# Performance work log

Measured on AMD Instinct MI355X. Metric: run time of the kernel, lower is better.

## Reference

```python
import jax, jax.numpy as jnp
from jax import lax
import numpy as np

EPS = 1e-5

def setup_inputs() -> dict:
    key = jax.random.key(0)
    k1, k2, k3, k4 = jax.random.split(key, 4)
    B, in_c, out_c, k, z_dim, H, W = 16, 128, 256, 3, 256, 64, 64
    fan_in = in_c * k * k
    x = jax.random.normal(k1, (B, in_c, H, W), dtype=jnp.float32)
    z = jax.random.normal(k2, (B, z_dim), dtype=jnp.float32)
    base_weight = jax.random.normal(k3, (out_c, in_c, k, k), dtype=jnp.float32) * np.sqrt(2.0 / fan_in)
    head_w = jax.random.normal(k4, (out_c * in_c * k * k, z_dim), dtype=jnp.float32) * np.sqrt(1.0 / z_dim)
    return {"x": x, "z": z, "base_weight": base_weight, "head_w": head_w}

def reference(x, z, base_weight, head_w):
    # x: [B, in_c, H, W]; z: [B, z_dim]; base_weight: [out_c, in_c, k, k]; head_w: [out_c*in_c*k*k, z_dim]
    B = x.shape[0]
    out_c, in_c, k, _ = base_weight.shape
    fan_in = in_c * k * k
    hyper_weight = 1.0

    # delta_w = Linear(z) -> [B, out_c, in_c, k, k]
    delta_w = jnp.einsum('bz,oz->bo', z, head_w).reshape(B, out_c, in_c, k, k)
    # standardize over (in_c, k, k) per (sample, out-channel)
    mu = jnp.mean(delta_w, axis=(2, 3, 4), keepdims=True)
    var = jnp.var(delta_w, axis=(2, 3, 4), keepdims=True)
    delta_w = (delta_w - mu) * lax.rsqrt(var + EPS)
    delta_w = delta_w * jnp.sqrt(2.0 / fan_in)

    w = (base_weight[None] + hyper_weight * delta_w) / jnp.sqrt(2.0)  # [B, out_c, in_c, k, k]

    pad = k // 2
    def conv_one(xb, wb):
        # xb: [in_c, H, W], wb: [out_c, in_c, k, k]
        return lax.conv_general_dilated(
            xb[None], wb, window_strides=(1, 1), padding=[(pad, pad), (pad, pad)],
            dimension_numbers=('NCHW', 'OIHW', 'NCHW'))[0]

    out = jax.vmap(conv_one)(x, w)  # [B, out_c, H_out, W_out]
    return out
```

## Files before the change

kernel.cpp:

```cpp
#include <hip/hip_runtime.h>

#define B_  16
#define IC  128
#define OC  256
#define ZD  256
#define HH  64
#define WW  64
#define FAN 1152
#define NO  294912
#define HP  66

typedef float    fvec4 __attribute__((ext_vector_type(4)));
typedef _Float16 f16x8 __attribute__((ext_vector_type(8)));
typedef _Float16 f16x4 __attribute__((ext_vector_type(4)));

__device__ __forceinline__ void gl_lds16(const _Float16* g, _Float16* ldst) {
  __builtin_amdgcn_global_load_lds(
      (const __attribute__((address_space(1))) unsigned int*)(const void*)g,
      (__attribute__((address_space(3))) unsigned int*)(void*)ldst,
      16, 0, 0);
}

__global__ __launch_bounds__(256) void delta_gemm_kernel(
    const float* __restrict__ z, const float* __restrict__ head_w,
    float* __restrict__ delta) {
  __shared__ _Float16 As[256 * 72];
  __shared__ _Float16 zsh[16 * 264];
  int t = threadIdx.x;
  int row0 = blockIdx.x * 256;
  int lane = t & 63, wave = t >> 6;
  int quad = lane >> 4, l16 = lane & 15;

  for (int u = t; u < 1024; u += 256) {
    int b = u >> 6, kq = u & 63;
    fvec4 v = *(const fvec4*)&z[b * 256 + kq * 4];
    f16x4 h = {(_Float16)v.x, (_Float16)v.y, (_Float16)v.z, (_Float16)v.w};
    *(f16x4*)&zsh[b * 264 + kq * 4] = h;
  }

  fvec4 acc[4];
#pragma unroll
  for (int i = 0; i < 4; ++i) acc[i] = (fvec4){0.f, 0.f, 0.f, 0.f};

  int srow_lo = t >> 4;
  int sseg = t & 15;

  for (int zc2 = 0; zc2 < 4; ++zc2) {
    __syncthreads();
#pragma unroll
    for (int i = 0; i < 16; ++i) {
      int row = i * 16 + srow_lo;
      fvec4 v = *(const fvec4*)&head_w[(size_t)(row0 + row) * 256 + zc2 * 64 + sseg * 4];
      f16x4 h = {(_Float16)v.x, (_Float16)v.y, (_Float16)v.z, (_Float16)v.w};
      *(f16x4*)&As[row * 72 + sseg * 4] = h;
    }
    __syncthreads();
#pragma unroll
    for (int kc = 0; kc < 2; ++kc) {
      f16x8 bfz = *(const f16x8*)&zsh[l16 * 264 + zc2 * 64 + kc * 32 + quad * 8];
#pragma unroll
      for (int mt = 0; mt < 4; ++mt) {
        f16x8 af = *(const f16x8*)&As[(wave * 64 + mt * 16 + l16) * 72 + kc * 32 + quad * 8];
        acc[mt] = __builtin_amdgcn_mfma_f32_16x16x32_f16(af, bfz, acc[mt], 0, 0, 0);
      }
    }
  }
#pragma unroll
  for (int mt = 0; mt < 4; ++mt) {
    int gr = row0 + wave * 64 + mt * 16 + quad * 4;
#pragma unroll
    for (int r = 0; r < 4; ++r)
      delta[(size_t)l16 * NO + gr + r] = acc[mt][r];
  }
}

__global__ __launch_bounds__(256) void standardize_kernel(
    const float* __restrict__ delta, const float* __restrict__ base_w,
    _Float16* __restrict__ w_h) {
  int b  = blockIdx.x >> 8;
  int oc = blockIdx.x & 255;
  int tid = threadIdx.x;
  const float* d = delta + (size_t)b * NO + oc * FAN;

  float s = 0.f, s2 = 0.f;
  for (int j = tid; j < FAN; j += 256) { float v = d[j]; s += v; s2 += v * v; }
#pragma unroll
  for (int off = 32; off > 0; off >>= 1) {
    s  += __shfl_down(s, off);
    s2 += __shfl_down(s2, off);
  }
  __shared__ float rs[4], rq[4];
  if ((tid & 63) == 0) { rs[tid >> 6] = s; rq[tid >> 6] = s2; }
  __syncthreads();
  float S  = rs[0] + rs[1] + rs[2] + rs[3];
  float S2 = rq[0] + rq[1] + rq[2] + rq[3];
  const float inv_fan = 1.0f / (float)FAN;
  float mu  = S * inv_fan;
  float var = S2 * inv_fan - mu * mu;
  const float inv_sqrt2 = 0.70710678118654752f;
  float sc = rsqrtf(var + 1e-5f) * sqrtf(2.0f / (float)FAN) * inv_sqrt2;

  const float* bw = base_w + oc * FAN;
  _Float16* wp = w_h + ((size_t)b * OC + oc) * FAN;
  for (int i = tid; i < FAN; i += 256) {
    int ic = i & 127, kk = i >> 7;
    int j = ic * 9 + kk;
    float val = bw[j] * inv_sqrt2 + (d[j] - mu) * sc;
    wp[i] = (_Float16)val;
  }
}

__global__ __launch_bounds__(256) void xpose_kernel(
    const float* __restrict__ x, _Float16* __restrict__ x_h) {
  int yp = blockIdx.x;
  int b  = blockIdx.y;
  int t  = threadIdx.x;
  _Float16* orow = x_h + ((size_t)(b * HP + yp)) * HP * IC;

  if (yp == 0 || yp == HP - 1) {
    fvec4 zz = (fvec4){0.f, 0.f, 0.f, 0.f};
    for (int u = t; u < HP * IC / 8; u += 256)
      ((fvec4*)orow)[u] = zz;
    return;
  }
  int y = yp - 1;
  __shared__ float tile[128 * 65];
#pragma unroll
  for (int i = 0; i < 8; ++i) {
    int F = i * 256 + t;
    int ic = F >> 4, xq = F & 15;
    fvec4 v = *(const fvec4*)&x[(((size_t)b * IC + ic) * HH + y) * WW + xq * 4];
    float* tp = &tile[ic * 65 + xq * 4];
    tp[0] = v.x; tp[1] = v.y; tp[2] = v.z; tp[3] = v.w;
  }
  __syncthreads();
#pragma unroll
  for (int j = 0; j < 4; ++j) {
    int u = j * 256 + t;
    int px = u >> 4, icg = u & 15;
    _Float16 h[8];
#pragma unroll
    for (int c = 0; c < 8; ++c) h[c] = (_Float16)tile[(icg * 8 + c) * 65 + px];
    *(f16x8*)&orow[(px + 1) * IC + icg * 8] = *(f16x8*)h;
  }
  if (t < 32) {
    int side = t >> 4, icg = t & 15;
    fvec4 zz = (fvec4){0.f, 0.f, 0.f, 0.f};
    *(fvec4*)&orow[(side ? (HP - 1) * IC : 0) + icg * 8] = zz;
  }
}

__global__ __launch_bounds__(256) void conv_mfma_kernel(
    const _Float16* __restrict__ x_h, const _Float16* __restrict__ w_h,
    float* __restrict__ out) {
  __shared__ __align__(16) _Float16 As[128 * 64];
  __shared__ __align__(16) _Float16 Bs[128 * 64];
  int t = threadIdx.x;
  int b = blockIdx.z;
  int oc0 = blockIdx.y * 128;
  int y0 = blockIdx.x * 2;
  int lane = t & 63, wave = t >> 6;
  int wm = wave >> 1, wn = wave & 1;
  int quad = lane >> 4, l16 = lane & 15;

  fvec4 acc[4][4];
#pragma unroll
  for (int i = 0; i < 4; ++i)
#pragma unroll
    for (int j = 0; j < 4; ++j) acc[i][j] = (fvec4){0.f, 0.f, 0.f, 0.f};

  int lrow = lane >> 3;
  int lseg = lane & 7;
  int sw   = lseg ^ lrow;

  const _Float16* apg[4];
#pragma unroll
  for (int n = 0; n < 4; ++n)
    apg[n] = w_h + ((size_t)(b * OC + oc0 + wave * 32 + n * 8 + lrow)) * FAN + sw * 8;

  const _Float16* bpg0 =
      x_h + (((size_t)(b * HP + y0 + (wave >> 1))) * HP + (wave & 1) * 32 + lrow) * IC + sw * 8;
  const _Float16* bpg1 = bpg0 + 16 * IC;

  _Float16* adst = As + wave * 32 * 64;
  _Float16* bdst = Bs + wave * 32 * 64;

  int s7 = l16 & 7;
  int arow = (wm * 64 + l16) * 64;
  int brow = (wn * 64 + l16) * 64;
  int aoff[2] = { arow + ((0 + quad) ^ s7) * 8, arow + ((4 + quad) ^ s7) * 8 };
  int boff[2] = { brow + ((0 + quad) ^ s7) * 8, brow + ((4 + quad) ^ s7) * 8 };

#pragma unroll
  for (int ky = 0; ky < 3; ++ky) {
#pragma unroll
    for (int kx = 0; kx < 3; ++kx) {
      const int kk = ky * 3 + kx;
      const _Float16* b0k = bpg0 + (ky * HP + kx) * IC;
      const _Float16* b1k = bpg1 + (ky * HP + kx) * IC;
#pragma unroll
      for (int icc = 0; icc < 2; ++icc) {
        __syncthreads();
#pragma unroll
        for (int n = 0; n < 4; ++n)
          gl_lds16(apg[n] + kk * 128 + icc * 64, adst + n * 512);
        gl_lds16(b0k + icc * 64,        bdst);
        gl_lds16(b0k + 1024 + icc * 64, bdst + 512);
        gl_lds16(b1k + icc * 64,        bdst + 1024);
        gl_lds16(b1k + 1024 + icc * 64, bdst + 1536);
        __syncthreads();
#pragma unroll
        for (int ks = 0; ks < 2; ++ks) {
          f16x8 af[4], bf[4];
#pragma unroll
          for (int i = 0; i < 4; ++i)
            af[i] = *(const f16x8*)&As[aoff[ks] + i * 1024];
#pragma unroll
          for (int j = 0; j < 4; ++j)
            bf[j] = *(const f16x8*)&Bs[boff[ks] + j * 1024];
#pragma unroll
          for (int i = 0; i < 4; ++i)
#pragma unroll
            for (int j = 0; j < 4; ++j)
              acc[i][j] = __builtin_amdgcn_mfma_f32_16x16x32_f16(af[i], bf[j], acc[i][j], 0, 0, 0);
        }
      }
    }
  }

#pragma unroll
  for (int i = 0; i < 4; ++i)
#pragma unroll
    for (int j = 0; j < 4; ++j) {
      int m  = oc0 + wm * 64 + i * 16 + quad * 4;
      int nn = wn * 64 + j * 16 + l16;
      int oy = y0 + (nn >> 6), ox = nn & 63;
      float* op = out + (((size_t)(b * OC + m) * HH + oy) * WW + ox);
#pragma unroll
      for (int r = 0; r < 4; ++r)
        op[(size_t)r * HH * WW] = acc[i][j][r];
    }
}

extern "C" void kernel_launch(void* const* d_in, const int* in_sizes, int n_in,
                              void* d_out, int out_size, void* d_ws, size_t ws_size,
                              hipStream_t stream) {
  const float* x      = (const float*)d_in[0];
  const float* z      = (const float*)d_in[1];
  const float* base_w = (const float*)d_in[2];
  const float* head_w = (const float*)d_in[3];
  float* out = (float*)d_out;

  _Float16* w_h   = (_Float16*)d_ws;
  float*    delta = (float*)((char*)d_ws + (size_t)B_ * OC * FAN * sizeof(_Float16));
  _Float16* x_h   = (_Float16*)((char*)d_ws + (size_t)B_ * OC * FAN * sizeof(_Float16)
                                            + (size_t)B_ * NO * sizeof(float));

  delta_gemm_kernel<<<NO / 256, 256, 0, stream>>>(z, head_w, delta);
  standardize_kernel<<<B_ * OC, 256, 0, stream>>>(delta, base_w, w_h);
  xpose_kernel<<<dim3(HP, B_), 256, 0, stream>>>(x, x_h);
  conv_mfma_kernel<<<dim3(32, 2, B_), 256, 0, stream>>>(x_h, w_h, out);
}
```

Before: 504.7 us.

## Rewrite conv kernel with 4-stage async LDS pipeline and 256x256 tiles

The conv kernel now uses 512 threads and computes a 256-oc by 256-pixel tile per block, with a K step of 32. Global-to-LDS loads are spread over four ring buffers and gated by manual vmcnt waits and a raw s_barrier, so loads are issued several stages ahead of the MFMAs. Wave priority is raised around the MFMA blocks. The aim is to hide memory latency and improve operand reuse. In exchange it uses more registers (32 accumulator tiles) and 128KB of LDS, and the launch grid shrinks to 256 blocks.

```diff
diff --git a/kernel.cpp b/kernel.cpp
--- a/kernel.cpp
+++ b/kernel.cpp
@@ -20,6 +20,12 @@
       (__attribute__((address_space(3))) unsigned int*)(void*)ldst,
       16, 0, 0);
 }
+
+#define BARRIER()  asm volatile("s_barrier" ::: "memory")
+#define WAITVM8()  asm volatile("s_waitcnt vmcnt(8)" ::: "memory")
+#define WAITVM4()  asm volatile("s_waitcnt vmcnt(4)" ::: "memory")
+#define WAITVM0()  asm volatile("s_waitcnt vmcnt(0)" ::: "memory")
+#define WAITLGKM() asm volatile("s_waitcnt lgkmcnt(0)" ::: "memory")
 
 __global__ __launch_bounds__(256) void delta_gemm_kernel(
     const float* __restrict__ z, const float* __restrict__ head_w,
@@ -150,95 +156,118 @@
   }
 }
 
-__global__ __launch_bounds__(256) void conv_mfma_kernel(
+__global__ __launch_bounds__(512, 2) void conv_mfma_kernel(
     const _Float16* __restrict__ x_h, const _Float16* __restrict__ w_h,
     float* __restrict__ out) {
-  __shared__ __align__(16) _Float16 As[128 * 64];
-  __shared__ __align__(16) _Float16 Bs[128 * 64];
-  int t = threadIdx.x;
-  int b = blockIdx.z;
-  int oc0 = blockIdx.y * 128;
-  int y0 = blockIdx.x * 2;
-  int lane = t & 63, wave = t >> 6;
-  int wm = wave >> 1, wn = wave & 1;
-  int quad = lane >> 4, l16 = lane & 15;
-
-  fvec4 acc[4][4];
-#pragma unroll
-  for (int i = 0; i < 4; ++i)
+  __shared__ __align__(16) _Float16 As[4 * 8192];
+  __shared__ __align__(16) _Float16 Bs[4 * 8192];
+  const int t = threadIdx.x;
+  const int b = blockIdx.y;
+  const int y0 = blockIdx.x * 4;
+  const int lane = t & 63, wave = t >> 6;
+  const int wm = wave >> 2, wn = wave & 3;
+  const int quad = lane >> 4, l16 = lane & 15;
+
+  fvec4 acc[8][4];
+#pragma unroll
+  for (int i = 0; i < 8; ++i)
 #pragma unroll
     for (int j = 0; j < 4; ++j) acc[i][j] = (fvec4){0.f, 0.f, 0.f, 0.f};
 
-  int lrow = lane >> 3;
-  int lseg = lane & 7;
-  int sw   = lseg ^ lrow;
-
-  const _Float16* apg[4];
-#pragma unroll
-  for (int n = 0; n < 4; ++n)
-    apg[n] = w_h + ((size_t)(b * OC + oc0 + wave * 32 + n * 8 + lrow)) * FAN + sw * 8;
-
-  const _Float16* bpg0 =
-      x_h + (((size_t)(b * HP + y0 + (wave >> 1))) * HP + (wave & 1) * 32 + lrow) * IC + sw * 8;
-  const _Float16* bpg1 = bpg0 + 16 * IC;
-
-  _Float16* adst = As + wave * 32 * 64;
-  _Float16* bdst = Bs + wave * 32 * 64;
-
-  int s7 = l16 & 7;
-  int arow = (wm * 64 + l16) * 64;
-  int brow = (wn * 64 + l16) * 64;
-  int aoff[2] = { arow + ((0 + quad) ^ s7) * 8, arow + ((4 + quad) ^ s7) * 8 };
-  int boff[2] = { brow + ((0 + quad) ^ s7) * 8, brow + ((4 + quad) ^ s7) * 8 };
-
-#pragma unroll
-  for (int ky = 0; ky < 3; ++ky) {
-#pragma unroll
-    for (int kx = 0; kx < 3; ++kx) {
-      const int kk = ky * 3 + kx;
-      const _Float16* b0k = bpg0 + (ky * HP + kx) * IC;
-      const _Float16* b1k = bpg1 + (ky * HP + kx) * IC;
-#pragma unroll
-      for (int icc = 0; icc < 2; ++icc) {
-        __syncthreads();
-#pragma unroll
-        for (int n = 0; n < 4; ++n)
-          gl_lds16(apg[n] + kk * 128 + icc * 64, adst + n * 512);
-        gl_lds16(b0k + icc * 64,        bdst);
-        gl_lds16(b0k + 1024 + icc * 64, bdst + 512);
-        gl_lds16(b1k + icc * 64,        bdst + 1024);
-        gl_lds16(b1k + 1024 + icc * 64, bdst + 1536);
-        __syncthreads();
-#pragma unroll
-        for (int ks = 0; ks < 2; ++ks) {
-          f16x8 af[4], bf[4];
-#pragma unroll
-          for (int i = 0; i < 4; ++i)
-            af[i] = *(const f16x8*)&As[aoff[ks] + i * 1024];
-#pragma unroll
-          for (int j = 0; j < 4; ++j)
-            bf[j] = *(const f16x8*)&Bs[boff[ks] + j * 1024];
-#pragma unroll
-          for (int i = 0; i < 4; ++i)
-#pragma unroll
-            for (int j = 0; j < 4; ++j)
-              acc[i][j] = __builtin_amdgcn_mfma_f32_16x16x32_f16(af[i], bf[j], acc[i][j], 0, 0, 0);
-        }
-      }
-    }
-  }
-
-#pragma unroll
-  for (int i = 0; i < 4; ++i)
-#pragma unroll
-    for (int j = 0; j < 4; ++j) {
-      int m  = oc0 + wm * 64 + i * 16 + quad * 4;
-      int nn = wn * 64 + j * 16 + l16;
-      int oy = y0 + (nn >> 6), ox = nn & 63;
-      float* op = out + (((size_t)(b * OC + m) * HH + oy) * WW + ox);
+  const int lr  = lane >> 2;
+  const int sw2 = (lane & 3) ^ ((lane >> 2) & 3) ^ ((lane >> 4) & 3);
+
+  const _Float16* apb0 = w_h + ((size_t)(b * OC + wave * 32 + lr)) * FAN + sw2 * 8;
+  const _Float16* apb1 = apb0 + (size_t)16 * FAN;
+  const int p0 = wave * 32 + lr, p1 = p0 + 16;
+  const _Float16* bpb0 =
+      x_h + (((size_t)(b * HP + y0 + (p0 >> 6))) * HP + (p0 & 63)) * IC + sw2 * 8;
+  const _Float16* bpb1 =
+      x_h + (((size_t)(b * HP + y0 + (p1 >> 6))) * HP + (p1 & 63)) * IC + sw2 * 8;
+
+  const int adst = wave * 32 * 32;
+
+  const int xoro = (l16 & 3) ^ ((l16 >> 2) & 3);
+  const int aro = (wm * 128 + l16) * 32 + ((quad ^ xoro) << 3);
+  const int bro = (wn * 64  + l16) * 32 + ((quad ^ xoro) << 3);
+
+#define STAGE(slot, akoff, bkoff)                                   \
+  do {                                                              \
+    _Float16* ad = As + (slot) * 8192 + adst;                       \
+    _Float16* bd = Bs + (slot) * 8192 + adst;                       \
+    gl_lds16(apb0 + (akoff), ad);                                   \
+    gl_lds16(apb1 + (akoff), ad + 512);                             \
+    gl_lds16(bpb0 + (bkoff), bd);                                   \
+    gl_lds16(bpb1 + (bkoff), bd + 512);                             \
+  } while (0)
+
+#define COMPUTE(slot)                                               \
+  do {                                                              \
+    const _Float16* Ab = As + (slot) * 8192;                        \
+    const _Float16* Bb = Bs + (slot) * 8192;                        \
+    f16x8 bf[4];                                                    \
+    _Pragma("unroll")                                               \
+    for (int nf = 0; nf < 4; ++nf)                                  \
+      bf[nf] = *(const f16x8*)&Bb[bro + nf * 512];                  \
+    __builtin_amdgcn_s_setprio(1);                                  \
+    _Pragma("unroll")                                               \
+    for (int mf = 0; mf < 8; ++mf) {                                \
+      f16x8 af = *(const f16x8*)&Ab[aro + mf * 512];                \
+      _Pragma("unroll")                                             \
+      for (int nf = 0; nf < 4; ++nf)                                \
+        acc[mf][nf] =                                               \
+            __builtin_amdgcn_mfma_f32_16x16x32_f16(af, bf[nf], acc[mf][nf], 0, 0, 0); \
+    }                                                               \
+    __builtin_amdgcn_s_setprio(0);                                  \
+  } while (0)
+
+  STAGE(0, 0, 0);
+  STAGE(1, 32, 32);
+  STAGE(2, 64, 64);
+
+  for (int kk = 0; kk < 8; ++kk) {
+    const int ky  = kk / 3,       kx  = kk % 3;
+    const int ky1 = (kk + 1) / 3, kx1 = (kk + 1) % 3;
+    const int ka  = kk * 128;
+    const int kb  = (ky * HP + kx) * IC;
+    const int ka1 = ka + 128;
+    const int kb1 = (ky1 * HP + kx1) * IC;
+#pragma unroll
+    for (int c = 0; c < 4; ++c) {
+      WAITLGKM();
+      WAITVM8();
+      BARRIER();
+      if (c == 0) STAGE(3, ka + 96, kb + 96);
+      else        STAGE(c - 1, ka1 + (c - 1) * 32, kb1 + (c - 1) * 32);
+      COMPUTE(c);
+    }
+  }
+  {
+    const int ka = 1024, kb = (2 * HP + 2) * IC;
+    WAITLGKM(); WAITVM8(); BARRIER();
+    STAGE(3, ka + 96, kb + 96);
+    COMPUTE(0);
+    WAITLGKM(); WAITVM8(); BARRIER();
+    COMPUTE(1);
+    WAITLGKM(); WAITVM4(); BARRIER();
+    COMPUTE(2);
+    WAITLGKM(); WAITVM0(); BARRIER();
+    COMPUTE(3);
+  }
+#undef STAGE
+#undef COMPUTE
+
+#pragma unroll
+  for (int mf = 0; mf < 8; ++mf)
+#pragma unroll
+    for (int nf = 0; nf < 4; ++nf) {
+      int oc = wm * 128 + mf * 16 + quad * 4;
+      int pn = wn * 64 + nf * 16 + l16;
+      int oy = y0 + (pn >> 6), ox = pn & 63;
+      float* op = out + (((size_t)(b * OC + oc) * HH + oy) * WW + ox);
 #pragma unroll
       for (int r = 0; r < 4; ++r)
-        op[(size_t)r * HH * WW] = acc[i][j][r];
+        op[(size_t)r * HH * WW] = acc[mf][nf][r];
     }
 }
 
@@ -259,5 +288,5 @@
   delta_gemm_kernel<<<NO / 256, 256, 0, stream>>>(z, head_w, delta);
   standardize_kernel<<<B_ * OC, 256, 0, stream>>>(delta, base_w, w_h);
   xpose_kernel<<<dim3(HP, B_), 256, 0, stream>>>(x, x_h);
-  conv_mfma_kernel<<<dim3(32, 2, B_), 256, 0, stream>>>(x_h, w_h, out);
-}
+  conv_mfma_kernel<<<dim3(16, B_), 512, 0, stream>>>(x_h, w_h, out);
+}
```

After: 509.5 us. No clear change (+0.9%).

## Fuse hypernetwork delta GEMM with per-channel standardization into one kernel

Applied to the files above, without the earlier changes.

Replaces the separate delta GEMM and standardize kernels with one kernel per output channel. Each block streams its head_w slice with register prefetch and double-buffered LDS, computes delta for all 16 samples via MFMA, reduces mean and variance in registers, and writes the fp16 standardized weights directly. This removes the fp32 delta buffer write and re-read and one launch. In exchange, only 256 large blocks run with heavy LDS use, which may limit memory-level parallelism when streaming head_w.

```diff
diff --git a/kernel.cpp b/kernel.cpp
--- a/kernel.cpp
+++ b/kernel.cpp
@@ -21,92 +21,118 @@
       16, 0, 0);
 }
 
-__global__ __launch_bounds__(256) void delta_gemm_kernel(
+#define BARRIER()  asm volatile("s_barrier" ::: "memory")
+#define WAITLGKM() asm volatile("s_waitcnt lgkmcnt(0)" ::: "memory")
+
+__global__ __launch_bounds__(512) void delta_std_fused_kernel(
     const float* __restrict__ z, const float* __restrict__ head_w,
-    float* __restrict__ delta) {
-  __shared__ _Float16 As[256 * 72];
+    const float* __restrict__ base_w, _Float16* __restrict__ w_h) {
+  __shared__ __align__(16) _Float16 As2[2][128 * 264];
   __shared__ _Float16 zsh[16 * 264];
-  int t = threadIdx.x;
-  int row0 = blockIdx.x * 256;
-  int lane = t & 63, wave = t >> 6;
-  int quad = lane >> 4, l16 = lane & 15;
-
-  for (int u = t; u < 1024; u += 256) {
+  __shared__ float bsh[FAN];
+  __shared__ float swS[8 * 16], swQ[8 * 16];
+  __shared__ float musb[16], scb[16];
+
+  const int t = threadIdx.x;
+  const int oc = blockIdx.x;
+  const int lane = t & 63, wave = t >> 6;
+  const int quad = lane >> 4, l16 = lane & 15;
+
+  const float* hw = head_w + (size_t)oc * FAN * ZD;
+  const float* hwp = hw + (size_t)wave * ZD + lane * 4;
+
+  fvec4 rg[16];
+#pragma unroll
+  for (int i = 0; i < 16; ++i)
+    rg[i] = *(const fvec4*)(hwp + (size_t)i * 8 * ZD);
+
+  for (int u = t; u < 1024; u += 512) {
     int b = u >> 6, kq = u & 63;
-    fvec4 v = *(const fvec4*)&z[b * 256 + kq * 4];
+    fvec4 v = *(const fvec4*)&z[b * ZD + kq * 4];
     f16x4 h = {(_Float16)v.x, (_Float16)v.y, (_Float16)v.z, (_Float16)v.w};
     *(f16x4*)&zsh[b * 264 + kq * 4] = h;
   }
-
-  fvec4 acc[4];
-#pragma unroll
-  for (int i = 0; i < 4; ++i) acc[i] = (fvec4){0.f, 0.f, 0.f, 0.f};
-
-  int srow_lo = t >> 4;
-  int sseg = t & 15;
-
-  for (int zc2 = 0; zc2 < 4; ++zc2) {
-    __syncthreads();
+  for (int u = t; u < FAN; u += 512) bsh[u] = base_w[oc * FAN + u];
+
+  fvec4 dd[9];
+
+#pragma unroll
+  for (int c = 0; c < 9; ++c) {
+    _Float16* dst = &As2[c & 1][wave * 264 + lane * 4];
 #pragma unroll
     for (int i = 0; i < 16; ++i) {
-      int row = i * 16 + srow_lo;
-      fvec4 v = *(const fvec4*)&head_w[(size_t)(row0 + row) * 256 + zc2 * 64 + sseg * 4];
+      fvec4 v = rg[i];
       f16x4 h = {(_Float16)v.x, (_Float16)v.y, (_Float16)v.z, (_Float16)v.w};
-      *(f16x4*)&As[row * 72 + sseg * 4] = h;
-    }
-    __syncthreads();
-#pragma unroll
-    for (int kc = 0; kc < 2; ++kc) {
-      f16x8 bfz = *(const f16x8*)&zsh[l16 * 264 + zc2 * 64 + kc * 32 + quad * 8];
-#pragma unroll
-      for (int mt = 0; mt < 4; ++mt) {
-        f16x8 af = *(const f16x8*)&As[(wave * 64 + mt * 16 + l16) * 72 + kc * 32 + quad * 8];
-        acc[mt] = __builtin_amdgcn_mfma_f32_16x16x32_f16(af, bfz, acc[mt], 0, 0, 0);
-      }
-    }
-  }
-#pragma unroll
-  for (int mt = 0; mt < 4; ++mt) {
-    int gr = row0 + wave * 64 + mt * 16 + quad * 4;
+      *(f16x4*)(dst + i * 8 * 264) = h;
+    }
+    if (c < 8) {
+      const float* src = hwp + (size_t)(c + 1) * 128 * ZD;
+#pragma unroll
+      for (int i = 0; i < 16; ++i)
+        rg[i] = *(const fvec4*)(src + (size_t)i * 8 * ZD);
+    }
+    WAITLGKM();
+    BARRIER();
+    fvec4 a = (fvec4){0.f, 0.f, 0.f, 0.f};
+    const _Float16* Ab = &As2[c & 1][(wave * 16 + l16) * 264 + quad * 8];
+    const _Float16* Zb = &zsh[l16 * 264 + quad * 8];
+#pragma unroll
+    for (int kc = 0; kc < 8; ++kc) {
+      f16x8 af = *(const f16x8*)(Ab + kc * 32);
+      f16x8 bz = *(const f16x8*)(Zb + kc * 32);
+      a = __builtin_amdgcn_mfma_f32_16x16x32_f16(af, bz, a, 0, 0, 0);
+    }
+    dd[c] = a;
+    WAITLGKM();
+    BARRIER();
+  }
+
+  float s = 0.f, s2 = 0.f;
+#pragma unroll
+  for (int c = 0; c < 9; ++c)
+#pragma unroll
+    for (int r = 0; r < 4; ++r) { float v = dd[c][r]; s += v; s2 += v * v; }
+  s  += __shfl_xor(s, 16);  s  += __shfl_xor(s, 32);
+  s2 += __shfl_xor(s2, 16); s2 += __shfl_xor(s2, 32);
+  if (lane < 16) { swS[wave * 16 + l16] = s; swQ[wave * 16 + l16] = s2; }
+  __syncthreads();
+  if (t < 16) {
+    float S = 0.f, S2 = 0.f;
+#pragma unroll
+    for (int w = 0; w < 8; ++w) { S += swS[w * 16 + t]; S2 += swQ[w * 16 + t]; }
+    const float inv_fan = 1.0f / (float)FAN;
+    float mu  = S * inv_fan;
+    float var = S2 * inv_fan - mu * mu;
+    const float inv_sqrt2 = 0.70710678118654752f;
+    musb[t] = mu;
+    scb[t]  = rsqrtf(var + 1e-5f) * sqrtf(2.0f / (float)FAN) * inv_sqrt2;
+  }
+  __syncthreads();
+
+  float* dsh = (float*)&As2[0][0];
+#pragma unroll
+  for (int c = 0; c < 9; ++c) {
+    int jb = c * 128 + wave * 16 + quad * 4;
 #pragma unroll
     for (int r = 0; r < 4; ++r)
-      delta[(size_t)l16 * NO + gr + r] = acc[mt][r];
-  }
-}
-
-__global__ __launch_bounds__(256) void standardize_kernel(
-    const float* __restrict__ delta, const float* __restrict__ base_w,
-    _Float16* __restrict__ w_h) {
-  int b  = blockIdx.x >> 8;
-  int oc = blockIdx.x & 255;
-  int tid = threadIdx.x;
-  const float* d = delta + (size_t)b * NO + oc * FAN;
-
-  float s = 0.f, s2 = 0.f;
-  for (int j = tid; j < FAN; j += 256) { float v = d[j]; s += v; s2 += v * v; }
-#pragma unroll
-  for (int off = 32; off > 0; off >>= 1) {
-    s  += __shfl_down(s, off);
-    s2 += __shfl_down(s2, off);
-  }
-  __shared__ float rs[4], rq[4];
-  if ((tid & 63) == 0) { rs[tid >> 6] = s; rq[tid >> 6] = s2; }
-  __syncthreads();
-  float S  = rs[0] + rs[1] + rs[2] + rs[3];
-  float S2 = rq[0] + rq[1] + rq[2] + rq[3];
-  const float inv_fan = 1.0f / (float)FAN;
-  float mu  = S * inv_fan;
-  float var = S2 * inv_fan - mu * mu;
+      dsh[(jb + r) * 17 + l16] = dd[c][r];
+  }
+  __syncthreads();
+
   const float inv_sqrt2 = 0.70710678118654752f;
-  float sc = rsqrtf(var + 1e-5f) * sqrtf(2.0f / (float)FAN) * inv_sqrt2;
-
-  const float* bw = base_w + oc * FAN;
-  _Float16* wp = w_h + ((size_t)b * OC + oc) * FAN;
-  for (int i = tid; i < FAN; i += 256) {
-    int ic = i & 127, kk = i >> 7;
-    int j = ic * 9 + kk;
-    float val = bw[j] * inv_sqrt2 + (d[j] - mu) * sc;
-    wp[i] = (_Float16)val;
+  for (int u = t; u < 2304; u += 512) {
+    int b = u / 144, seg = u % 144;
+    int p0 = seg * 8;
+    int kk = p0 >> 7, ic0 = p0 & 127;
+    float mu = musb[b], sc = scb[b];
+    _Float16 h[8];
+#pragma unroll
+    for (int e = 0; e < 8; ++e) {
+      int j = (ic0 + e) * 9 + kk;
+      float val = bsh[j] * inv_sqrt2 + (dsh[j * 17 + b] - mu) * sc;
+      h[e] = (_Float16)val;
+    }
+    *(f16x8*)&w_h[((size_t)b * OC + oc) * FAN + p0] = *(f16x8*)h;
   }
 }
 
@@ -251,13 +277,10 @@
   const float* head_w = (const float*)d_in[3];
   float* out = (float*)d_out;
 
-  _Float16* w_h   = (_Float16*)d_ws;
-  float*    delta = (float*)((char*)d_ws + (size_t)B_ * OC * FAN * sizeof(_Float16));
-  _Float16* x_h   = (_Float16*)((char*)d_ws + (size_t)B_ * OC * FAN * sizeof(_Float16)
-                                            + (size_t)B_ * NO * sizeof(float));
-
-  delta_gemm_kernel<<<NO / 256, 256, 0, stream>>>(z, head_w, delta);
-  standardize_kernel<<<B_ * OC, 256, 0, stream>>>(delta, base_w, w_h);
+  _Float16* w_h = (_Float16*)d_ws;
+  _Float16* x_h = (_Float16*)((char*)d_ws + (size_t)B_ * OC * FAN * sizeof(_Float16));
+
+  delta_std_fused_kernel<<<OC, 512, 0, stream>>>(z, head_w, base_w, w_h);
   xpose_kernel<<<dim3(HP, B_), 256, 0, stream>>>(x, x_h);
   conv_mfma_kernel<<<dim3(32, 2, B_), 256, 0, stream>>>(x_h, w_h, out);
 }
```

Result: faster. 487.6 us (-3.4%).
